# Optimization experiments

Hardware: AMD Instinct MI355X
Metric: run time of the kernel (lower is better)

## Reference

```python
import jax, jax.numpy as jnp
import numpy as np

DIM = 512
HEADS = 16
WS = (2, 7, 7)
N = WS[0] * WS[1] * WS[2]  # 98
NW = 64  # number of windows in mask
B_ = 512  # num_windows * batch
HEAD_DIM = DIM // HEADS
SCALE = HEAD_DIM ** -0.5
TABLE = (2 * WS[0] - 1) * (2 * WS[1] - 1) * (2 * WS[2] - 1)  # 507


def _relative_position_index():
    # Faithful to the repo (note: middle coord is NOT multiplied by (2*Ww-1),
    # matching the source exactly).
    ct, ch, cw = np.arange(WS[0]), np.arange(WS[1]), np.arange(WS[2])
    coords = np.stack(np.meshgrid(ct, ch, cw, indexing='ij'))  # [3,Th,Tw,Tw]
    flat = coords.reshape(3, -1)  # [3,N]
    rel = flat[:, :, None] - flat[:, None, :]  # [3,N,N]
    rel = rel.transpose(1, 2, 0).copy()  # [N,N,3]
    rel[:, :, 0] += WS[0] - 1
    rel[:, :, 1] += WS[1] - 1
    rel[:, :, 2] += WS[2] - 1
    rel[:, :, 0] *= (2 * WS[1] - 1) * (2 * WS[2] - 1)
    return rel.sum(-1).astype(np.int32)  # [N,N]


def setup_inputs() -> dict:
    key = jax.random.key(0)
    ks = jax.random.split(key, 7)
    x = jax.random.normal(ks[0], (B_, N, DIM), dtype=jnp.float32)
    mask = jnp.zeros((NW, N, N), dtype=jnp.float32)
    qkv_w = jax.random.normal(ks[1], (3 * DIM, DIM), dtype=jnp.float32) * (DIM ** -0.5)
    qkv_b = jnp.zeros((3 * DIM,), dtype=jnp.float32)
    proj_w = jax.random.normal(ks[2], (DIM, DIM), dtype=jnp.float32) * (DIM ** -0.5)
    proj_b = jnp.zeros((DIM,), dtype=jnp.float32)
    bias_table = jax.random.normal(ks[3], (TABLE, HEADS), dtype=jnp.float32) * 0.02
    rel_index = jnp.asarray(_relative_position_index())
    return {"x": x, "mask": mask, "qkv_w": qkv_w, "qkv_b": qkv_b,
            "proj_w": proj_w, "proj_b": proj_b, "bias_table": bias_table,
            "rel_index": rel_index}


def reference(x, mask, qkv_w, qkv_b, proj_w, proj_b, bias_table, rel_index):
    Bw, n, c = x.shape
    # QKV projection -> [3, B_, H, N, hd]
    qkv = (x @ qkv_w.T + qkv_b).reshape(Bw, n, 3, HEADS, HEAD_DIM)
    qkv = qkv.transpose(2, 0, 3, 1, 4)
    q, k, v = qkv[0], qkv[1], qkv[2]
    attn = jnp.einsum('bhnd,bhmd->bhnm', q * SCALE, k)  # [B_,H,N,N]
    # Gathered relative position bias -> [H,N,N]
    bias = bias_table[rel_index.reshape(-1)].reshape(n, n, HEADS).transpose(2, 0, 1)
    attn = attn + bias[None]
    # Broadcast mask over batch groups of nW windows
    nW = mask.shape[0]
    attn = attn.reshape(Bw // nW, nW, HEADS, n, n) + mask[None, :, None]
    attn = attn.reshape(Bw, HEADS, n, n)
    attn = jax.nn.softmax(attn, axis=-1)
    out = jnp.einsum('bhnm,bhmd->bhnd', attn, v)
    out = out.transpose(0, 2, 1, 3).reshape(Bw, n, c)
    return out @ proj_w.T + proj_b
```

## Files before the change

kernel.cpp:

```cpp
#include <hip/hip_runtime.h>
#include <stdint.h>

#define HEADS 16
#define NTOK 98
#define HD 32
#define SCALE_Q 0.17677669529663687f

typedef __attribute__((ext_vector_type(4))) float floatx4;
typedef __attribute__((ext_vector_type(8))) short shortx8;

__device__ __forceinline__ unsigned short f2bf(float f) {
  union { float f; unsigned u; } v; v.f = f;
  unsigned r = v.u + 0x7fffu + ((v.u >> 16) & 1u);
  return (unsigned short)(r >> 16);
}
__device__ __forceinline__ float bf2f(unsigned short s) {
  union { unsigned u; float f; } v; v.u = ((unsigned)s) << 16;
  return v.f;
}

__device__ __forceinline__ void gload_lds16(const void* g, void* l) {
  __builtin_amdgcn_global_load_lds(
      (const __attribute__((address_space(1))) unsigned int*)g,
      (__attribute__((address_space(3))) unsigned int*)l, 16, 0, 0);
}

__global__ void convert_x_kernel(const float* __restrict__ x,
                                 unsigned short* __restrict__ xbf) {
  int idx = blockIdx.x * 256 + threadIdx.x;
  const float4 f0 = *(const float4*)(x + (size_t)idx * 8);
  const float4 f1 = *(const float4*)(x + (size_t)idx * 8 + 4);
  union { ushort us[8]; uint4 u4; } pk;
  pk.us[0] = f2bf(f0.x); pk.us[1] = f2bf(f0.y);
  pk.us[2] = f2bf(f0.z); pk.us[3] = f2bf(f0.w);
  pk.us[4] = f2bf(f1.x); pk.us[5] = f2bf(f1.y);
  pk.us[6] = f2bf(f1.z); pk.us[7] = f2bf(f1.w);
  *(uint4*)(xbf + (size_t)idx * 8) = pk.u4;
}

__global__ void convert_w_kernel(const float* __restrict__ qkv_w,
                                 const float* __restrict__ proj_w,
                                 unsigned short* __restrict__ wq,
                                 unsigned short* __restrict__ wp) {
  int idx = blockIdx.x * 256 + threadIdx.x;
  if (idx < 1536 * 512) wq[idx] = f2bf(qkv_w[idx]);
  if (idx < 512 * 512) wp[idx] = f2bf(proj_w[idx]);
}

__global__ void bm_kernel(const float* __restrict__ table,
                          const int* __restrict__ rel,
                          const float* __restrict__ mask,
                          unsigned short* __restrict__ bm) {
  int ij = blockIdx.x * 256 + threadIdx.x;
  int wh = blockIdx.y;
  int w = wh >> 4, h = wh & 15;
  if (ij < NTOK * NTOK) {
    float v = table[rel[ij] * HEADS + h] + mask[w * (NTOK * NTOK) + ij];
    bm[(size_t)wh * (NTOK * NTOK) + ij] = f2bf(v);
  }
}

__global__ __launch_bounds__(256, 2)
void qkv_gemm_kernel(const unsigned short* __restrict__ xbf,
                     const unsigned short* __restrict__ wbf,
                     const float* __restrict__ qkv_b,
                     unsigned short* __restrict__ q_out,
                     unsigned short* __restrict__ k_out,
                     unsigned short* __restrict__ v_out) {
  __shared__ unsigned short As[128 * 32];
  __shared__ unsigned short Bs[256 * 32];
  const int tid = threadIdx.x;
  const int wave = tid >> 6, lane = tid & 63;
  const int m0 = blockIdx.x * 128, n0 = blockIdx.y * 256;
  const int wm = wave & 1, wn = wave >> 1;
  const int ln15 = lane & 15, qd = lane >> 4;
  const int bl_r = lane >> 2, bl_s = lane & 3;

  floatx4 acc[4][8] = {};

  for (int k0 = 0; k0 < 512; k0 += 32) {
#pragma unroll
    for (int c = 0; c < 2; ++c) {
      int rbase = wave * 32 + c * 16;
      const unsigned short* g =
          xbf + (size_t)(m0 + rbase + bl_r) * 512 + k0 + bl_s * 8;
      gload_lds16((const void*)g, (void*)&As[rbase * 32]);
    }
#pragma unroll
    for (int c = 0; c < 4; ++c) {
      int rbase = wave * 64 + c * 16;
      const unsigned short* g =
          wbf + (size_t)(n0 + rbase + bl_r) * 512 + k0 + bl_s * 8;
      gload_lds16((const void*)g, (void*)&Bs[rbase * 32]);
    }
    __syncthreads();

    shortx8 afrag[4], bfrag[8];
#pragma unroll
    for (int mt = 0; mt < 4; ++mt)
      afrag[mt] = *(const shortx8*)&As[(wm * 64 + mt * 16 + ln15) * 32 + qd * 8];
#pragma unroll
    for (int nt = 0; nt < 8; ++nt)
      bfrag[nt] = *(const shortx8*)&Bs[(wn * 128 + nt * 16 + ln15) * 32 + qd * 8];
#pragma unroll
    for (int mt = 0; mt < 4; ++mt)
#pragma unroll
      for (int nt = 0; nt < 8; ++nt)
        acc[mt][nt] = __builtin_amdgcn_mfma_f32_16x16x32_bf16(
            afrag[mt], bfrag[nt], acc[mt][nt], 0, 0, 0);
    __syncthreads();
  }

#pragma unroll
  for (int mt = 0; mt < 4; ++mt) {
#pragma unroll
    for (int r = 0; r < 4; ++r) {
      int grow = m0 + wm * 64 + mt * 16 + qd * 4 + r;
      unsigned b = (unsigned)grow / 98u;
      unsigned i = (unsigned)grow - b * 98u;
#pragma unroll
      for (int nt = 0; nt < 8; ++nt) {
        int col = n0 + wn * 128 + nt * 16 + ln15;
        float val = acc[mt][nt][r] + qkv_b[col];
        int which = col >> 9;
        int h = (col >> 5) & 15;
        int d = col & 31;
        size_t oidx = ((size_t)(b * 16 + h) * 98 + i) * 32 + d;
        if (which == 0)      q_out[oidx] = f2bf(val * SCALE_Q);
        else if (which == 1) k_out[oidx] = f2bf(val);
        else                 v_out[oidx] = f2bf(val);
      }
    }
  }
}

__global__ __launch_bounds__(256, 6)
void attn_kernel(const unsigned short* __restrict__ qg,
                 const unsigned short* __restrict__ kg,
                 const unsigned short* __restrict__ vg,
                 const unsigned short* __restrict__ bmg,
                 unsigned short* __restrict__ outg) {
  __shared__ unsigned short Vt[32 * 136];
  __shared__ unsigned short Ps[4][16 * 40];
  const int tid = threadIdx.x;
  const int bh = blockIdx.x;
  const int b = bh >> 4, h = bh & 15, w = b & 63;
  const size_t base = (size_t)bh * (NTOK * HD);
  const int wave = tid >> 6, lane = tid & 63;
  const int ln15 = lane & 15, qd = lane >> 4;
  const unsigned short* bmh = bmg + (size_t)(w * 16 + h) * (NTOK * NTOK);

  for (int idx = tid; idx < 544; idx += 256)
    ((uint4*)Vt)[idx] = make_uint4(0, 0, 0, 0);
  __syncthreads();
  for (int t = tid; t < 392; t += 256) {
    int i = t >> 2, seg = t & 3;
    union { uint4 u4; unsigned short us[8]; } u;
    u.u4 = *(const uint4*)(vg + base + i * 32 + seg * 8);
    int d0 = seg * 8;
#pragma unroll
    for (int e = 0; e < 8; ++e) Vt[(d0 + e) * 136 + i] = u.us[e];
  }
  __syncthreads();

  floatx4 oacc[2];
#pragma unroll
  for (int mslot = 0; mslot < 2; ++mslot) {
    int mt = wave + mslot * 4;
    if (mt >= 7) break;
    shortx8 af = *(const shortx8*)(qg + base + (mt * 16 + ln15) * 32 + qd * 8);
    float s[7][4];
    {
      floatx4 sacc[7];
#pragma unroll
      for (int nt = 0; nt < 7; ++nt) {
        shortx8 bf = *(const shortx8*)(kg + base + (nt * 16 + ln15) * 32 + qd * 8);
        floatx4 z = {};
        sacc[nt] = __builtin_amdgcn_mfma_f32_16x16x32_bf16(af, bf, z, 0, 0, 0);
      }
#pragma unroll
      for (int r = 0; r < 4; ++r) {
        int i = mt * 16 + qd * 4 + r;
        int ii = i < 97 ? i : 97;
#pragma unroll
        for (int nt = 0; nt < 7; ++nt) {
          int j = nt * 16 + ln15;
          int jj = j < 97 ? j : 97;
          float bmv = bf2f(bmh[ii * NTOK + jj]);
          s[nt][r] = (i < NTOK && j < NTOK) ? sacc[nt][r] + bmv : -1e30f;
        }
      }
    }
    float linv[4];
#pragma unroll
    for (int r = 0; r < 4; ++r) {
      float mx = s[0][r];
#pragma unroll
      for (int nt = 1; nt < 7; ++nt) mx = fmaxf(mx, s[nt][r]);
#pragma unroll
      for (int off = 1; off < 16; off <<= 1)
        mx = fmaxf(mx, __shfl_xor(mx, off, 64));
      float sum = 0.f;
#pragma unroll
      for (int nt = 0; nt < 7; ++nt) {
        float p = __expf(s[nt][r] - mx);
        s[nt][r] = p;
        sum += p;
      }
#pragma unroll
      for (int off = 1; off < 16; off <<= 1) sum += __shfl_xor(sum, off, 64);
      linv[r] = 1.0f / sum;
    }
    oacc[0] = (floatx4){};
    oacc[1] = (floatx4){};
#pragma unroll
    for (int ks = 0; ks < 4; ++ks) {
#pragma unroll
      for (int nt2 = 0; nt2 < 2; ++nt2) {
        int nt = ks * 2 + nt2;
#pragma unroll
        for (int r = 0; r < 4; ++r)
          Ps[wave][(qd * 4 + r) * 40 + nt2 * 16 + ln15] = f2bf(s[nt][r]);
      }
      shortx8 ap = *(const shortx8*)&Ps[wave][ln15 * 40 + qd * 8];
      shortx8 bv0 = *(const shortx8*)&Vt[ln15 * 136 + ks * 32 + qd * 8];
      shortx8 bv1 = *(const shortx8*)&Vt[(16 + ln15) * 136 + ks * 32 + qd * 8];
      oacc[0] = __builtin_amdgcn_mfma_f32_16x16x32_bf16(ap, bv0, oacc[0], 0, 0, 0);
      oacc[1] = __builtin_amdgcn_mfma_f32_16x16x32_bf16(ap, bv1, oacc[1], 0, 0, 0);
    }
#pragma unroll
    for (int r = 0; r < 4; ++r) {
      int i = mt * 16 + qd * 4 + r;
      if (i < NTOK) {
        size_t ob = ((size_t)b * NTOK + i) * 512 + h * 32;
#pragma unroll
        for (int vt = 0; vt < 2; ++vt)
          outg[ob + vt * 16 + ln15] = f2bf(oacc[vt][r] * linv[r]);
      }
    }
  }
}

__global__ __launch_bounds__(256, 2)
void proj_gemm_kernel(const unsigned short* __restrict__ a,
                      const unsigned short* __restrict__ wbf,
                      const float* __restrict__ proj_b,
                      float* __restrict__ out) {
  __shared__ unsigned short As[128 * 32];
  __shared__ unsigned short Bs[128 * 32];
  const int tid = threadIdx.x;
  const int wave = tid >> 6, lane = tid & 63;
  const int m0 = blockIdx.x * 128, n0 = blockIdx.y * 128;
  const int wm = wave & 1, wn = wave >> 1;
  const int ln15 = lane & 15, qd = lane >> 4;
  const int bl_r = lane >> 2, bl_s = lane & 3;

  floatx4 acc[4][4] = {};

  for (int k0 = 0; k0 < 512; k0 += 32) {
#pragma unroll
    for (int c = 0; c < 2; ++c) {
      int rbase = wave * 32 + c * 16;
      const unsigned short* ga =
          a + (size_t)(m0 + rbase + bl_r) * 512 + k0 + bl_s * 8;
      gload_lds16((const void*)ga, (void*)&As[rbase * 32]);
      const unsigned short* gb =
          wbf + (size_t)(n0 + rbase + bl_r) * 512 + k0 + bl_s * 8;
      gload_lds16((const void*)gb, (void*)&Bs[rbase * 32]);
    }
    __syncthreads();

    shortx8 afrag[4], bfrag[4];
#pragma unroll
    for (int mt = 0; mt < 4; ++mt)
      afrag[mt] = *(const shortx8*)&As[(wm * 64 + mt * 16 + ln15) * 32 + qd * 8];
#pragma unroll
    for (int nt = 0; nt < 4; ++nt)
      bfrag[nt] = *(const shortx8*)&Bs[(wn * 64 + nt * 16 + ln15) * 32 + qd * 8];
#pragma unroll
    for (int mt = 0; mt < 4; ++mt)
#pragma unroll
      for (int nt = 0; nt < 4; ++nt)
        acc[mt][nt] = __builtin_amdgcn_mfma_f32_16x16x32_bf16(
            afrag[mt], bfrag[nt], acc[mt][nt], 0, 0, 0);
    __syncthreads();
  }

#pragma unroll
  for (int mt = 0; mt < 4; ++mt) {
#pragma unroll
    for (int r = 0; r < 4; ++r) {
      int grow = m0 + wm * 64 + mt * 16 + qd * 4 + r;
#pragma unroll
      for (int nt = 0; nt < 4; ++nt) {
        int col = n0 + wn * 64 + nt * 16 + ln15;
        out[(size_t)grow * 512 + col] = acc[mt][nt][r] + proj_b[col];
      }
    }
  }
}

extern "C" void kernel_launch(void* const* d_in, const int* in_sizes, int n_in,
                              void* d_out, int out_size, void* d_ws, size_t ws_size,
                              hipStream_t stream) {
  const float* x          = (const float*)d_in[0];
  const float* mask       = (const float*)d_in[1];
  const float* qkv_w      = (const float*)d_in[2];
  const float* qkv_b      = (const float*)d_in[3];
  const float* proj_w     = (const float*)d_in[4];
  const float* proj_b     = (const float*)d_in[5];
  const float* bias_table = (const float*)d_in[6];
  const int*   rel_index  = (const int*)d_in[7];
  float* out = (float*)d_out;

  char* ws = (char*)d_ws;
  unsigned short* ws_qkvw  = (unsigned short*)(ws + 0);
  unsigned short* ws_projw = (unsigned short*)(ws + 1572864);
  unsigned short* ws_bm    = (unsigned short*)(ws + 2097152);
  unsigned short* ws_q     = (unsigned short*)(ws + 21766144);
  unsigned short* ws_k     = (unsigned short*)(ws + 73146368);
  unsigned short* ws_v     = (unsigned short*)(ws + 124526592);
  unsigned short* ws_attn  = (unsigned short*)(ws + 175906816);
  unsigned short* ws_xbf   = ws_attn;

  hipLaunchKernelGGL(convert_x_kernel, dim3(12544), dim3(256), 0, stream,
                     x, ws_xbf);
  hipLaunchKernelGGL(convert_w_kernel, dim3(3072), dim3(256), 0, stream,
                     qkv_w, proj_w, ws_qkvw, ws_projw);
  hipLaunchKernelGGL(bm_kernel, dim3(38, 1024), dim3(256), 0, stream,
                     bias_table, rel_index, mask, ws_bm);
  hipLaunchKernelGGL(qkv_gemm_kernel, dim3(392, 6), dim3(256), 0, stream,
                     ws_xbf, ws_qkvw, qkv_b, ws_q, ws_k, ws_v);
  hipLaunchKernelGGL(attn_kernel, dim3(8192), dim3(256), 0, stream,
                     ws_q, ws_k, ws_v, ws_bm, ws_attn);
  hipLaunchKernelGGL(proj_gemm_kernel, dim3(392, 4), dim3(256), 0, stream,
                     ws_attn, ws_projw, proj_b, out);
}
```

Baseline: 521.3 us.

## Double-buffer and swizzle LDS in QKV and projection GEMMs with 512-thread blocks

Both GEMM kernels now use 8 waves per block and double-buffered LDS tiles, so the next K-slice is prefetched while MFMAs run on the current one. LDS layout gains an XOR swizzle on the 16-byte chunk index to reduce bank conflicts on fragment reads. The projection GEMM grows to 128x256 tiles with half as many column blocks. This adds LDS use per block and register pressure under the new launch bounds, which may limit occupancy.

Result: faster. 495.6 us (-4.9%).

```diff
diff --git a/kernel.cpp b/kernel.cpp
--- a/kernel.cpp
+++ b/kernel.cpp
@@ -60,15 +60,15 @@
   }
 }
 
-__global__ __launch_bounds__(256, 2)
+__global__ __launch_bounds__(512, 4)
 void qkv_gemm_kernel(const unsigned short* __restrict__ xbf,
                      const unsigned short* __restrict__ wbf,
                      const float* __restrict__ qkv_b,
                      unsigned short* __restrict__ q_out,
                      unsigned short* __restrict__ k_out,
                      unsigned short* __restrict__ v_out) {
-  __shared__ unsigned short As[128 * 32];
-  __shared__ unsigned short Bs[256 * 32];
+  __shared__ unsigned short As[2][128 * 32];
+  __shared__ unsigned short Bs[2][256 * 32];
   const int tid = threadIdx.x;
   const int wave = tid >> 6, lane = tid & 63;
   const int m0 = blockIdx.x * 128, n0 = blockIdx.y * 256;
@@ -76,39 +76,49 @@
   const int ln15 = lane & 15, qd = lane >> 4;
   const int bl_r = lane >> 2, bl_s = lane & 3;
 
-  floatx4 acc[4][8] = {};
-
+  const int sg_st = bl_s ^ ((bl_r >> 1) & 3);
+  const int swz_rd = (qd ^ ((ln15 >> 1) & 3)) * 8;
+
+  const int a_row = wave * 16 + bl_r;
+  const unsigned short* aG = xbf + (size_t)(m0 + a_row) * 512 + sg_st * 8;
+  const int b_row0 = wave * 32 + bl_r;
+  const unsigned short* bG0 = wbf + (size_t)(n0 + b_row0) * 512 + sg_st * 8;
+  const unsigned short* bG1 = wbf + (size_t)(n0 + b_row0 + 16) * 512 + sg_st * 8;
+
+  floatx4 acc[4][4] = {};
+
+  gload_lds16((const void*)aG, (void*)&As[0][wave * 16 * 32]);
+  gload_lds16((const void*)bG0, (void*)&Bs[0][wave * 32 * 32]);
+  gload_lds16((const void*)bG1, (void*)&Bs[0][(wave * 32 + 16) * 32]);
+  __syncthreads();
+
+  int cur = 0;
+#pragma unroll 2
   for (int k0 = 0; k0 < 512; k0 += 32) {
-#pragma unroll
-    for (int c = 0; c < 2; ++c) {
-      int rbase = wave * 32 + c * 16;
-      const unsigned short* g =
-          xbf + (size_t)(m0 + rbase + bl_r) * 512 + k0 + bl_s * 8;
-      gload_lds16((const void*)g, (void*)&As[rbase * 32]);
-    }
-#pragma unroll
-    for (int c = 0; c < 4; ++c) {
-      int rbase = wave * 64 + c * 16;
-      const unsigned short* g =
-          wbf + (size_t)(n0 + rbase + bl_r) * 512 + k0 + bl_s * 8;
-      gload_lds16((const void*)g, (void*)&Bs[rbase * 32]);
-    }
-    __syncthreads();
-
-    shortx8 afrag[4], bfrag[8];
+    if (k0 + 32 < 512) {
+      int nx = cur ^ 1;
+      gload_lds16((const void*)(aG + k0 + 32), (void*)&As[nx][wave * 16 * 32]);
+      gload_lds16((const void*)(bG0 + k0 + 32), (void*)&Bs[nx][wave * 32 * 32]);
+      gload_lds16((const void*)(bG1 + k0 + 32),
+                  (void*)&Bs[nx][(wave * 32 + 16) * 32]);
+    }
+    shortx8 afrag[4], bfrag[4];
 #pragma unroll
     for (int mt = 0; mt < 4; ++mt)
-      afrag[mt] = *(const shortx8*)&As[(wm * 64 + mt * 16 + ln15) * 32 + qd * 8];
-#pragma unroll
-    for (int nt = 0; nt < 8; ++nt)
-      bfrag[nt] = *(const shortx8*)&Bs[(wn * 128 + nt * 16 + ln15) * 32 + qd * 8];
+      afrag[mt] =
+          *(const shortx8*)&As[cur][(wm * 64 + mt * 16 + ln15) * 32 + swz_rd];
+#pragma unroll
+    for (int nt = 0; nt < 4; ++nt)
+      bfrag[nt] =
+          *(const shortx8*)&Bs[cur][(wn * 64 + nt * 16 + ln15) * 32 + swz_rd];
 #pragma unroll
     for (int mt = 0; mt < 4; ++mt)
 #pragma unroll
-      for (int nt = 0; nt < 8; ++nt)
+      for (int nt = 0; nt < 4; ++nt)
         acc[mt][nt] = __builtin_amdgcn_mfma_f32_16x16x32_bf16(
             afrag[mt], bfrag[nt], acc[mt][nt], 0, 0, 0);
     __syncthreads();
+    cur ^= 1;
   }
 
 #pragma unroll
@@ -119,8 +129,8 @@
       unsigned b = (unsigned)grow / 98u;
       unsigned i = (unsigned)grow - b * 98u;
 #pragma unroll
-      for (int nt = 0; nt < 8; ++nt) {
-        int col = n0 + wn * 128 + nt * 16 + ln15;
+      for (int nt = 0; nt < 4; ++nt) {
+        int col = n0 + wn * 64 + nt * 16 + ln15;
         float val = acc[mt][nt][r] + qkv_b[col];
         int which = col >> 9;
         int h = (col >> 5) & 15;
@@ -241,42 +251,55 @@
   }
 }
 
-__global__ __launch_bounds__(256, 2)
+__global__ __launch_bounds__(512, 4)
 void proj_gemm_kernel(const unsigned short* __restrict__ a,
                       const unsigned short* __restrict__ wbf,
                       const float* __restrict__ proj_b,
                       float* __restrict__ out) {
-  __shared__ unsigned short As[128 * 32];
-  __shared__ unsigned short Bs[128 * 32];
+  __shared__ unsigned short As[2][128 * 32];
+  __shared__ unsigned short Bs[2][256 * 32];
   const int tid = threadIdx.x;
   const int wave = tid >> 6, lane = tid & 63;
-  const int m0 = blockIdx.x * 128, n0 = blockIdx.y * 128;
+  const int m0 = blockIdx.x * 128, n0 = blockIdx.y * 256;
   const int wm = wave & 1, wn = wave >> 1;
   const int ln15 = lane & 15, qd = lane >> 4;
   const int bl_r = lane >> 2, bl_s = lane & 3;
 
+  const int sg_st = bl_s ^ ((bl_r >> 1) & 3);
+  const int swz_rd = (qd ^ ((ln15 >> 1) & 3)) * 8;
+
+  const int a_row = wave * 16 + bl_r;
+  const unsigned short* aG = a + (size_t)(m0 + a_row) * 512 + sg_st * 8;
+  const int b_row0 = wave * 32 + bl_r;
+  const unsigned short* bG0 = wbf + (size_t)(n0 + b_row0) * 512 + sg_st * 8;
+  const unsigned short* bG1 = wbf + (size_t)(n0 + b_row0 + 16) * 512 + sg_st * 8;
+
   floatx4 acc[4][4] = {};
 
+  gload_lds16((const void*)aG, (void*)&As[0][wave * 16 * 32]);
+  gload_lds16((const void*)bG0, (void*)&Bs[0][wave * 32 * 32]);
+  gload_lds16((const void*)bG1, (void*)&Bs[0][(wave * 32 + 16) * 32]);
+  __syncthreads();
+
+  int cur = 0;
+#pragma unroll 2
   for (int k0 = 0; k0 < 512; k0 += 32) {
-#pragma unroll
-    for (int c = 0; c < 2; ++c) {
-      int rbase = wave * 32 + c * 16;
-      const unsigned short* ga =
-          a + (size_t)(m0 + rbase + bl_r) * 512 + k0 + bl_s * 8;
-      gload_lds16((const void*)ga, (void*)&As[rbase * 32]);
-      const unsigned short* gb =
-          wbf + (size_t)(n0 + rbase + bl_r) * 512 + k0 + bl_s * 8;
-      gload_lds16((const void*)gb, (void*)&Bs[rbase * 32]);
-    }
-    __syncthreads();
-
+    if (k0 + 32 < 512) {
+      int nx = cur ^ 1;
+      gload_lds16((const void*)(aG + k0 + 32), (void*)&As[nx][wave * 16 * 32]);
+      gload_lds16((const void*)(bG0 + k0 + 32), (void*)&Bs[nx][wave * 32 * 32]);
+      gload_lds16((const void*)(bG1 + k0 + 32),
+                  (void*)&Bs[nx][(wave * 32 + 16) * 32]);
+    }
     shortx8 afrag[4], bfrag[4];
 #pragma unroll
     for (int mt = 0; mt < 4; ++mt)
-      afrag[mt] = *(const shortx8*)&As[(wm * 64 + mt * 16 + ln15) * 32 + qd * 8];
+      afrag[mt] =
+          *(const shortx8*)&As[cur][(wm * 64 + mt * 16 + ln15) * 32 + swz_rd];
 #pragma unroll
     for (int nt = 0; nt < 4; ++nt)
-      bfrag[nt] = *(const shortx8*)&Bs[(wn * 64 + nt * 16 + ln15) * 32 + qd * 8];
+      bfrag[nt] =
+          *(const shortx8*)&Bs[cur][(wn * 64 + nt * 16 + ln15) * 32 + swz_rd];
 #pragma unroll
     for (int mt = 0; mt < 4; ++mt)
 #pragma unroll
@@ -284,6 +307,7 @@
         acc[mt][nt] = __builtin_amdgcn_mfma_f32_16x16x32_bf16(
             afrag[mt], bfrag[nt], acc[mt][nt], 0, 0, 0);
     __syncthreads();
+    cur ^= 1;
   }
 
 #pragma unroll
@@ -329,10 +353,10 @@
                      qkv_w, proj_w, ws_qkvw, ws_projw);
   hipLaunchKernelGGL(bm_kernel, dim3(38, 1024), dim3(256), 0, stream,
                      bias_table, rel_index, mask, ws_bm);
-  hipLaunchKernelGGL(qkv_gemm_kernel, dim3(392, 6), dim3(256), 0, stream,
+  hipLaunchKernelGGL(qkv_gemm_kernel, dim3(392, 6), dim3(512), 0, stream,
                      ws_xbf, ws_qkvw, qkv_b, ws_q, ws_k, ws_v);
   hipLaunchKernelGGL(attn_kernel, dim3(8192), dim3(256), 0, stream,
                      ws_q, ws_k, ws_v, ws_bm, ws_attn);
-  hipLaunchKernelGGL(proj_gemm_kernel, dim3(392, 4), dim3(256), 0, stream,
+  hipLaunchKernelGGL(proj_gemm_kernel, dim3(392, 2), dim3(512), 0, stream,
                      ws_attn, ws_projw, proj_b, out);
 }
```
